# Kernel tuning notes

Measured on AMD Instinct MI355X. Metric: run time of the kernel, lower is better.

The kernel has to match this reference:

```python
import jax, jax.numpy as jnp
import numpy as np

# ---- fixed sizes ----
N_IN = 100_000          # total inner nodes
NODES_PER_INNER = 50    # nodes per inner graph
N_OUT = N_IN // NODES_PER_INNER          # 2000 outer nodes (= num inner graphs)
NODES_PER_OUTER = 125   # outer nodes per outer graph
B = N_OUT // NODES_PER_OUTER             # 16 graphs in the batch
DEG = 8
E_IN = N_IN * DEG        # 800_000 inner edges
E_OUT = N_OUT * DEG      # 16_000 outer edges
IN_FEATS = 64
OUT_FEATS = 64
H = 128                  # h_feats = [128]*6
NUM_CLASSES = 10


def _rand_edges(key, n_graphs, nodes_per_graph, edges_per_graph):
    """Random edges that stay inside each graph of a batched graph."""
    k1, k2 = jax.random.split(key)
    src_l = jax.random.randint(k1, (n_graphs, edges_per_graph), 0, nodes_per_graph)
    dst_l = jax.random.randint(k2, (n_graphs, edges_per_graph), 0, nodes_per_graph)
    off = (jnp.arange(n_graphs) * nodes_per_graph)[:, None]
    return ((src_l + off).reshape(-1).astype(jnp.int32),
            (dst_l + off).reshape(-1).astype(jnp.int32))


def setup_inputs() -> dict:
    key = jax.random.key(0)
    ks = jax.random.split(key, 24)
    inner_src, inner_dst = _rand_edges(ks[0], N_OUT, NODES_PER_INNER, E_IN // N_OUT)
    outer_src, outer_dst = _rand_edges(ks[1], B, NODES_PER_OUTER, E_OUT // B)

    def w(k, fan_in, fan_out):
        return jax.random.normal(k, (fan_in, fan_out), jnp.float32) * (1.0 / np.sqrt(fan_in))

    inp = {
        "in_layer_feat": jax.random.normal(ks[2], (N_IN, IN_FEATS), jnp.float32),
        "out_layer_feat": jax.random.normal(ks[3], (N_OUT, OUT_FEATS), jnp.float32),
        "inner_ew": jax.random.uniform(ks[4], (E_IN,), jnp.float32) + 0.5,
        "outer_ew": jax.random.uniform(ks[5], (E_OUT,), jnp.float32) + 0.5,
        "W1": w(ks[6], IN_FEATS, H),        "b1": jnp.zeros((H,), jnp.float32),
        "W2": w(ks[7], H, H),               "b2": jnp.zeros((H,), jnp.float32),
        "W3": w(ks[8], OUT_FEATS + H, H),   "b3": jnp.zeros((H,), jnp.float32),
        "W4": w(ks[9], H, H),               "b4": jnp.zeros((H,), jnp.float32),
        "W5": w(ks[10], H, H),              "b5": jnp.zeros((H,), jnp.float32),
        "W6": w(ks[11], H, H),              "b6": jnp.zeros((H,), jnp.float32),
        "Wc": w(ks[12], H, NUM_CLASSES),    "bc": jnp.zeros((NUM_CLASSES,), jnp.float32),
        "inner_src": inner_src, "inner_dst": inner_dst,
        "outer_src": outer_src, "outer_dst": outer_dst,
        "inner_node_graph": (jnp.arange(N_IN) // NODES_PER_INNER).astype(jnp.int32),
        "outer_node_graph": (jnp.arange(N_OUT) // NODES_PER_OUTER).astype(jnp.int32),
    }
    return inp


def graph_conv(src, dst, ew, x, W, b, n_nodes):
    """DGL GraphConv, norm='both', weighted aggregation, zero-in-degree allowed."""
    ones = jnp.ones(src.shape[0], x.dtype)
    deg_out = jnp.clip(jax.ops.segment_sum(ones, src, num_segments=n_nodes), 1.0)
    deg_in = jnp.clip(jax.ops.segment_sum(ones, dst, num_segments=n_nodes), 1.0)
    xs = x * jax.lax.rsqrt(deg_out)[:, None]                      # src normalization
    msg = xs[src] * ew[:, None]                                   # u_mul_e
    agg = jax.ops.segment_sum(msg, dst, num_segments=n_nodes)     # copy_e -> sum
    agg = agg * jax.lax.rsqrt(deg_in)[:, None]                    # dst normalization
    return agg @ W + b


def mean_nodes(h, node_graph, n_graphs, nodes_per_graph):
    return jax.ops.segment_sum(h, node_graph, num_segments=n_graphs) / nodes_per_graph


def reference(in_layer_feat, out_layer_feat, inner_ew, outer_ew,
              W1, b1, W2, b2, W3, b3, W4, b4, W5, b5, W6, b6, Wc, bc,
              inner_src, inner_dst, outer_src, outer_dst,
              inner_node_graph, outer_node_graph):
    # inner-graph message passing
    h = jax.nn.relu(graph_conv(inner_src, inner_dst, inner_ew, in_layer_feat, W1, b1, N_IN))
    h = jax.nn.relu(graph_conv(inner_src, inner_dst, inner_ew, h, W2, b2, N_IN))
    reduced = mean_nodes(h, inner_node_graph, N_OUT, float(NODES_PER_INNER))  # [N_OUT, H]
    merged = jnp.concatenate([out_layer_feat, reduced], axis=-1)              # [N_OUT, OUT_FEATS+H]
    # outer-graph message passing
    h = jax.nn.relu(graph_conv(outer_src, outer_dst, outer_ew, merged, W3, b3, N_OUT))
    h = jax.nn.relu(graph_conv(outer_src, outer_dst, outer_ew, h, W4, b4, N_OUT))
    h = jax.nn.relu(graph_conv(outer_src, outer_dst, outer_ew, h, W5, b5, N_OUT))
    h = jax.nn.relu(graph_conv(outer_src, outer_dst, outer_ew, h, W6, b6, N_OUT))
    hg = mean_nodes(h, outer_node_graph, B, float(NODES_PER_OUTER))           # [B, H]
    return hg @ Wc + bc                                                       # [B, NUM_CLASSES]
```

## Files before the change

kernel.cpp:

```cpp
#include <hip/hip_runtime.h>

#define NPI 50
#define EPI 400
#define NPO 125
#define EPO 1000
#define N_IN 100000
#define N_OUT 2000
#define NB 16
#define NC 10

typedef _Float16 half_t;
typedef _Float16 f16x8 __attribute__((ext_vector_type(8)));
typedef float f32x4 __attribute__((ext_vector_type(4)));

#define MFMA(a, b, c) __builtin_amdgcn_mfma_f32_16x16x32_f16(a, b, c, 0, 0, 0)

__device__ __forceinline__ void lds_barrier() {
    asm volatile("s_waitcnt lgkmcnt(0)" ::: "memory");
    __builtin_amdgcn_s_barrier();
}

__device__ __forceinline__ f16x8 lds_ld8(const half_t* base, int row, int k, int strideB) {
    return *(const f16x8*)((const char*)base + row * strideB + ((k * 2) ^ ((row & 7) << 4)));
}
__device__ __forceinline__ void lds_st1(half_t* base, int row, int col, int strideB, float v) {
    *(half_t*)((char*)base + row * strideB + ((col * 2) ^ ((row & 7) << 4))) = (half_t)v;
}
__device__ __forceinline__ void lds_st1h(half_t* base, int row, int col, int strideB, half_t v) {
    *(half_t*)((char*)base + row * strideB + ((col * 2) ^ ((row & 7) << 4))) = v;
}
__device__ __forceinline__ f16x8 scr_ld8(const half_t* base, int row, int k) {
    return *(const f16x8*)((const char*)base + row * 64 + ((k * 2) ^ ((row & 3) << 4)));
}
__device__ __forceinline__ void scr_st1(half_t* base, int row, int col, float v) {
    *(half_t*)((char*)base + row * 64 + ((col * 2) ^ ((row & 3) << 4))) = (half_t)v;
}

__global__ __launch_bounds__(256) void k_pre(
    const float* __restrict__ W1, const float* __restrict__ W2,
    const float* __restrict__ W3, const float* __restrict__ W4,
    const float* __restrict__ W5, const float* __restrict__ W6,
    half_t* __restrict__ WT1, half_t* __restrict__ WT2,
    half_t* __restrict__ WT3, half_t* __restrict__ WT4,
    half_t* __restrict__ WT5, half_t* __restrict__ WT6,
    const float* __restrict__ ew, const int* __restrict__ esrc,
    const int* __restrict__ edst, half_t* __restrict__ Aout)
{
    __shared__ float Af[NPO * NPO];
    __shared__ int cO[NPO], cI[NPO];
    __shared__ float rso[NPO], rsi[NPO];
    const int t = threadIdx.x;

    if (blockIdx.x < 384) {
        int i = blockIdx.x * 256 + t;
        const float* src; half_t* dst; int K;
        if      (i < 8192)  { src = W1; dst = WT1; K = 64; }
        else if (i < 24576) { src = W2; dst = WT2; K = 128; i -= 8192; }
        else if (i < 49152) { src = W3; dst = WT3; K = 192; i -= 24576; }
        else if (i < 65536) { src = W4; dst = WT4; K = 128; i -= 49152; }
        else if (i < 81920) { src = W5; dst = WT5; K = 128; i -= 65536; }
        else                { src = W6; dst = WT6; K = 128; i -= 81920; }
        int c = i & 127, k = i >> 7;
        dst[c * K + k] = (half_t)src[k * 128 + c];
        return;
    }

    const int g = blockIdx.x - 384;
    const int nb = g * NPO, eb = g * EPO;
    for (int i = t; i < NPO * NPO; i += 256) Af[i] = 0.f;
    if (t < NPO) { cO[t] = 0; cI[t] = 0; }
    __syncthreads();
    for (int e = t; e < EPO; e += 256) {
        int s = esrc[eb + e] - nb, d = edst[eb + e] - nb;
        atomicAdd(&Af[d * NPO + s], ew[eb + e]);
        atomicAdd(&cO[s], 1); atomicAdd(&cI[d], 1);
    }
    __syncthreads();
    if (t < NPO) {
        rso[t] = rsqrtf((float)max(cO[t], 1));
        rsi[t] = rsqrtf((float)max(cI[t], 1));
    }
    __syncthreads();
    for (int i = t; i < 128 * 16; i += 256) {
        int d = i >> 4, s0 = (i & 15) * 8;
        f16x8 v;
        #pragma unroll
        for (int j = 0; j < 8; j++) {
            int s = s0 + j;
            float x = (d < NPO && s < NPO) ? Af[d * NPO + s] * rsi[d] * rso[s] : 0.f;
            v[j] = (half_t)x;
        }
        *(f16x8*)&Aout[(size_t)g * 16384 + d * 128 + s0] = v;
    }
}

__global__ __launch_bounds__(256, 5) void k_inner(
    const float* __restrict__ X, const float* __restrict__ outfeat,
    const float* __restrict__ ew, const int* __restrict__ esrc,
    const int* __restrict__ edst,
    const half_t* __restrict__ WT1, const float* __restrict__ b1,
    const half_t* __restrict__ WT2, const float* __restrict__ b2,
    half_t* __restrict__ merged)
{
    __shared__ alignas(16) char smem[21504];
    half_t* R2  = (half_t*)smem;
    float*  Af  = (float*)smem;
    half_t* scr = (half_t*)(smem + 16384);
    float*  pool= (float*)(smem + 20480);
    int*    cO  = (int*)(smem + 20992);
    int*    cI  = (int*)(smem + 21248);

    const int g = blockIdx.x, t = threadIdx.x;
    const int w = t >> 6, l = t & 63, lr = l & 15, lk = l >> 4;
    const int nb = g * NPI, eb = g * EPI;
    half_t* scrw = scr + w * 512;

    float ofv = (t < 64) ? outfeat[(size_t)g * 64 + t] : 0.f;
    int s0e, d0e; float w0e;
    { int e = eb + t; s0e = esrc[e] - nb; d0e = edst[e] - nb; w0e = ew[e]; }
    int s1e = 0, d1e = 0; float w1e = 0.f;
    const bool e1v = (t + 256 < EPI);
    if (e1v) { int e = eb + t + 256; s1e = esrc[e] - nb; d1e = edst[e] - nb; w1e = ew[e]; }
    const int srow = t >> 2, qc = t & 3;
    f16x8 xh0 = {}, xh1 = {};
    if (srow < NPI) {
        const float* xp = &X[(size_t)(nb + srow) * 64 + qc * 16];
        float4 a = *(const float4*)(xp + 0), b = *(const float4*)(xp + 4);
        float4 c = *(const float4*)(xp + 8), d = *(const float4*)(xp + 12);
        xh0[0]=(half_t)a.x; xh0[1]=(half_t)a.y; xh0[2]=(half_t)a.z; xh0[3]=(half_t)a.w;
        xh0[4]=(half_t)b.x; xh0[5]=(half_t)b.y; xh0[6]=(half_t)b.z; xh0[7]=(half_t)b.w;
        xh1[0]=(half_t)c.x; xh1[1]=(half_t)c.y; xh1[2]=(half_t)c.z; xh1[3]=(half_t)c.w;
        xh1[4]=(half_t)d.x; xh1[5]=(half_t)d.y; xh1[6]=(half_t)d.z; xh1[7]=(half_t)d.w;
    }

    if (t < 64) { cO[t] = 0; cI[t] = 0; }
    if (t >= 64 && t < 192) pool[t - 64] = 0.f;
    for (int i = t; i < 4096; i += 256) Af[i] = 0.f;
    lds_barrier();

    atomicAdd(&Af[d0e * 64 + (s0e ^ ((d0e & 7) << 2))], w0e);
    atomicAdd(&cO[s0e], 1); atomicAdd(&cI[d0e], 1);
    if (e1v) {
        atomicAdd(&Af[d1e * 64 + (s1e ^ ((d1e & 7) << 2))], w1e);
        atomicAdd(&cO[s1e], 1); atomicAdd(&cI[d1e], 1);
    }
    lds_barrier();

    f16x8 afr[2];
    {
        const int r = w * 16 + lr;
        const int sw = (r & 7) << 2;
        const float rsi_l = rsqrtf((float)max(cI[r], 1));
        #pragma unroll
        for (int ks = 0; ks < 2; ks++) {
            const int c0 = ks * 32 + lk * 8;
            f32x4 v0 = *(const f32x4*)&Af[r * 64 + (c0 ^ sw)];
            f32x4 v1 = *(const f32x4*)&Af[r * 64 + ((c0 + 4) ^ sw)];
            f16x8 fr;
            #pragma unroll
            for (int j = 0; j < 4; j++)
                fr[j] = (half_t)(v0[j] * rsi_l * rsqrtf((float)max(cO[c0 + j], 1)));
            #pragma unroll
            for (int j = 0; j < 4; j++)
                fr[4 + j] = (half_t)(v1[j] * rsi_l * rsqrtf((float)max(cO[c0 + 4 + j], 1)));
            afr[ks] = fr;
        }
    }
    lds_barrier();

    #pragma unroll
    for (int i = 0; i < 8; i++) lds_st1h(R2, qc * 16 + i, srow, 128, xh0[i]);
    #pragma unroll
    for (int i = 0; i < 8; i++) lds_st1h(R2, qc * 16 + 8 + i, srow, 128, xh1[i]);
    lds_barrier();

    f32x4 hacc[8] = {};
    #pragma unroll
    for (int kf = 0; kf < 2; kf++) {
        f16x8 wb[8];
        #pragma unroll
        for (int nt = 0; nt < 8; nt++)
            wb[nt] = *(const f16x8*)&WT1[(nt * 16 + lr) * 64 + kf * 32 + lk * 8];
        #pragma unroll
        for (int j = 0; j < 2; j++) {
            const int ft = kf * 2 + j;
            f32x4 tacc = {};
            #pragma unroll
            for (int ks = 0; ks < 2; ks++) {
                f16x8 b = lds_ld8(R2, ft * 16 + lr, ks * 32 + lk * 8, 128);
                tacc = MFMA(afr[ks], b, tacc);
            }
            #pragma unroll
            for (int q = 0; q < 4; q++) scr_st1(scrw, lk * 4 + q, j * 16 + lr, tacc[q]);
        }
        f16x8 a1 = scr_ld8(scrw, lr, lk * 8);
        #pragma unroll
        for (int nt = 0; nt < 8; nt++) hacc[nt] = MFMA(a1, wb[nt], hacc[nt]);
    }
    lds_barrier();
    #pragma unroll
    for (int nt = 0; nt < 8; nt++) {
        int c = nt * 16 + lr;
        float bb = b1[c];
        #pragma unroll
        for (int q = 0; q < 4; q++)
            lds_st1(R2, c, w * 16 + lk * 4 + q, 128, fmaxf(hacc[nt][q] + bb, 0.f));
    }
    lds_barrier();

    f32x4 h2[8] = {};
    #pragma unroll
    for (int kf = 0; kf < 4; kf++) {
        f16x8 wb[8];
        #pragma unroll
        for (int nt = 0; nt < 8; nt++)
            wb[nt] = *(const f16x8*)&WT2[(nt * 16 + lr) * 128 + kf * 32 + lk * 8];
        #pragma unroll
        for (int j = 0; j < 2; j++) {
            const int ft = kf * 2 + j;
            f32x4 tacc = {};
            #pragma unroll
            for (int ks = 0; ks < 2; ks++) {
                f16x8 b = lds_ld8(R2, ft * 16 + lr, ks * 32 + lk * 8, 128);
                tacc = MFMA(afr[ks], b, tacc);
            }
            #pragma unroll
            for (int q = 0; q < 4; q++) scr_st1(scrw, lk * 4 + q, j * 16 + lr, tacc[q]);
        }
        f16x8 a1 = scr_ld8(scrw, lr, lk * 8);
        #pragma unroll
        for (int nt = 0; nt < 8; nt++) h2[nt] = MFMA(a1, wb[nt], h2[nt]);
    }
    #pragma unroll
    for (int nt = 0; nt < 8; nt++) {
        int c = nt * 16 + lr;
        float bb = b2[c];
        float ps = 0.f;
        #pragma unroll
        for (int q = 0; q < 4; q++) {
            int m = w * 16 + lk * 4 + q;
            float v = fmaxf(h2[nt][q] + bb, 0.f);
            ps += (m < NPI) ? v : 0.f;
        }
        ps += __shfl_xor(ps, 16);
        ps += __shfl_xor(ps, 32);
        if (lk == 0) atomicAdd(&pool[c], ps);
    }
    lds_barrier();
    if (t < 64) merged[(size_t)g * 192 + t] = (half_t)ofv;
    else if (t < 192) merged[(size_t)g * 192 + t] = (half_t)(pool[t - 64] * (1.f / NPI));
}

template <int FIN, bool STAGE, bool LAST>
__device__ __forceinline__ void outer_layer(
    const f16x8* afr, const half_t* __restrict__ mg,
    const half_t* __restrict__ WT, const float* __restrict__ bias,
    half_t* bufP, half_t* bufQ, float* pool,
    int wr, int wc, int lr, int lk, int t)
{
    f32x4 hacc[4] = {};
    constexpr int NCH = FIN / 64;
    f16x8 hv[NCH];
    if constexpr (STAGE) {
        const int s = t >> 3, fo = (t & 7) * 8;
        #pragma unroll
        for (int ch = 0; ch < NCH; ch++) {
            f16x8 z = {};
            hv[ch] = (s < NPO) ? *(const f16x8*)&mg[(size_t)s * 192 + ch * 64 + fo] : z;
        }
    }
    #pragma unroll
    for (int ch = 0; ch < NCH; ch++) {
        f16x8 wtb[8];
        #pragma unroll
        for (int ks2 = 0; ks2 < 2; ks2++)
            #pragma unroll
            for (int nt = 0; nt < 4; nt++)
                wtb[ks2 * 4 + nt] = *(const f16x8*)&WT[
                    (size_t)(wc * 64 + nt * 16 + lr) * FIN + ch * 64 + ks2 * 32 + lk * 8];
        if constexpr (STAGE) {
            const int s = t >> 3, fo = (t & 7) * 8;
            #pragma unroll
            for (int j = 0; j < 8; j++) lds_st1h(bufP, fo + j, s, 256, hv[ch][j]);
            lds_barrier();
        }
        const int rb = STAGE ? 0 : ch * 64;
        f32x4 tacc[2] = {};
        #pragma unroll
        for (int ks = 0; ks < 4; ks++) {
            #pragma unroll
            for (int nt = 0; nt < 2; nt++) {
                f16x8 b = lds_ld8(bufP, rb + wc * 32 + nt * 16 + lr, ks * 32 + lk * 8, 256);
                tacc[nt] = MFMA(afr[ks], b, tacc[nt]);
            }
        }
        #pragma unroll
        for (int nt = 0; nt < 2; nt++)
            #pragma unroll
            for (int q = 0; q < 4; q++)
                lds_st1(bufQ, wr * 16 + lk * 4 + q, wc * 32 + nt * 16 + lr, 128,
                        tacc[nt][q]);
        lds_barrier();
        #pragma unroll
        for (int ks2 = 0; ks2 < 2; ks2++) {
            f16x8 a1 = lds_ld8(bufQ, wr * 16 + lr, ks2 * 32 + lk * 8, 128);
            #pragma unroll
            for (int nt = 0; nt < 4; nt++)
                hacc[nt] = MFMA(a1, wtb[ks2 * 4 + nt], hacc[nt]);
        }
        lds_barrier();
    }
    if constexpr (!LAST) {
        #pragma unroll
        for (int nt = 0; nt < 4; nt++) {
            int c = wc * 64 + nt * 16 + lr;
            float bb = bias[c];
            #pragma unroll
            for (int q = 0; q < 4; q++)
                lds_st1(bufP, c, wr * 16 + lk * 4 + q, 256, fmaxf(hacc[nt][q] + bb, 0.f));
        }
        lds_barrier();
    } else {
        #pragma unroll
        for (int nt = 0; nt < 4; nt++) {
            int c = wc * 64 + nt * 16 + lr;
            float bb = bias[c];
            float ps = 0.f;
            #pragma unroll
            for (int q = 0; q < 4; q++) {
                int d = wr * 16 + lk * 4 + q;
                float v = fmaxf(hacc[nt][q] + bb, 0.f);
                ps += (d < NPO) ? v : 0.f;
            }
            ps += __shfl_xor(ps, 16);
            ps += __shfl_xor(ps, 32);
            if (lk == 0) atomicAdd(&pool[c], ps);
        }
        lds_barrier();
    }
}

__global__ __launch_bounds__(1024) void k_outer(
    const half_t* __restrict__ Aout, const half_t* __restrict__ merged,
    const half_t* __restrict__ WT3, const float* __restrict__ b3,
    const half_t* __restrict__ WT4, const float* __restrict__ b4,
    const half_t* __restrict__ WT5, const float* __restrict__ b5,
    const half_t* __restrict__ WT6, const float* __restrict__ b6,
    const float* __restrict__ Wc, const float* __restrict__ bc,
    float* __restrict__ out)
{
    __shared__ alignas(16) char smem[49704];
    half_t* bufP = (half_t*)smem;
    half_t* bufQ = (half_t*)(smem + 32768);
    float*  pool = (float*)(smem + 49152);
    float*  cls  = (float*)(smem + 49664);

    const int g = blockIdx.x, t = threadIdx.x;
    const int w = t >> 6, l = t & 63, lr = l & 15, lk = l >> 4;
    const int wr = w & 7, wc = w >> 3;
    const half_t* mg = merged + (size_t)g * NPO * 192;

    f16x8 afr[4];
    #pragma unroll
    for (int ks = 0; ks < 4; ks++)
        afr[ks] = *(const f16x8*)&Aout[(size_t)g * 16384
                                       + (wr * 16 + lr) * 128 + ks * 32 + lk * 8];
    if (t < 128) pool[t] = 0.f;
    if (t >= 128 && t < 128 + NC) cls[t - 128] = 0.f;
    lds_barrier();

    outer_layer<192, true,  false>(afr, mg, WT3, b3, bufP, bufQ, pool, wr, wc, lr, lk, t);
    outer_layer<128, false, false>(afr, nullptr, WT4, b4, bufP, bufQ, pool, wr, wc, lr, lk, t);
    outer_layer<128, false, false>(afr, nullptr, WT5, b5, bufP, bufQ, pool, wr, wc, lr, lk, t);
    outer_layer<128, false, true >(afr, nullptr, WT6, b6, bufP, bufQ, pool, wr, wc, lr, lk, t);

    if (t < 128) {
        float val = pool[t] * (1.f / NPO);
        float p[NC];
        #pragma unroll
        for (int c = 0; c < NC; c++) p[c] = val * Wc[t * NC + c];
        #pragma unroll
        for (int off = 32; off >= 1; off >>= 1)
            #pragma unroll
            for (int c = 0; c < NC; c++) p[c] += __shfl_xor(p[c], off);
        if ((t & 63) == 0)
            #pragma unroll
            for (int c = 0; c < NC; c++) atomicAdd(&cls[c], p[c]);
    }
    lds_barrier();
    if (t < NC) out[g * NC + t] = cls[t] + bc[t];
}

extern "C" void kernel_launch(void* const* d_in, const int* in_sizes, int n_in,
                              void* d_out, int out_size, void* d_ws, size_t ws_size,
                              hipStream_t stream)
{
    const float* X       = (const float*)d_in[0];
    const float* outfeat = (const float*)d_in[1];
    const float* iew     = (const float*)d_in[2];
    const float* oew     = (const float*)d_in[3];
    const float* W1 = (const float*)d_in[4];  const float* b1 = (const float*)d_in[5];
    const float* W2 = (const float*)d_in[6];  const float* b2 = (const float*)d_in[7];
    const float* W3 = (const float*)d_in[8];  const float* b3 = (const float*)d_in[9];
    const float* W4 = (const float*)d_in[10]; const float* b4 = (const float*)d_in[11];
    const float* W5 = (const float*)d_in[12]; const float* b5 = (const float*)d_in[13];
    const float* W6 = (const float*)d_in[14]; const float* b6 = (const float*)d_in[15];
    const float* Wc = (const float*)d_in[16]; const float* bc = (const float*)d_in[17];
    const int* isrc = (const int*)d_in[18];   const int* idst = (const int*)d_in[19];
    const int* osrc = (const int*)d_in[20];   const int* odst = (const int*)d_in[21];

    char* base = (char*)d_ws;
    half_t* WT1 = (half_t*)(base + 0);
    half_t* WT2 = (half_t*)(base + 16384);
    half_t* WT3 = (half_t*)(base + 49152);
    half_t* WT4 = (half_t*)(base + 98304);
    half_t* WT5 = (half_t*)(base + 131072);
    half_t* WT6 = (half_t*)(base + 163840);
    half_t* AoutG  = (half_t*)(base + 196608);
    half_t* merged = (half_t*)(base + 720896);

    k_pre<<<400, 256, 0, stream>>>(W1, W2, W3, W4, W5, W6,
                                   WT1, WT2, WT3, WT4, WT5, WT6,
                                   oew, osrc, odst, AoutG);
    k_inner<<<N_OUT, 256, 0, stream>>>(X, outfeat, iew, isrc, idst,
                                       WT1, b1, WT2, b2, merged);
    k_outer<<<NB, 1024, 0, stream>>>(AoutG, merged, WT3, b3, WT4, b4,
                                     WT5, b5, WT6, b6, Wc, bc, (float*)d_out);
}
```

Before: 122.0 us.

## Split outer-graph stage into per-layer multi-block kernels with transposed activations

Replaces the single outer-graph kernel, which ran 16 blocks of 1024 threads over all four layers, with four per-layer kernels of 128 single-wave blocks plus a small pooling and classifier kernel. Each block handles a 16-row slice of one outer graph and reads the previous layer's transposed fp16 activations from global memory. The inner kernel now writes the merged features in this transposed per-graph layout. The aim is to spread the outer stage across many more compute units instead of 16. The cost is four extra kernel launches, global round-trips between layers, and padding columns of the transposed merged buffer that are never initialised.

```diff
diff --git a/kernel.cpp b/kernel.cpp
--- a/kernel.cpp
+++ b/kernel.cpp
@@ -29,11 +29,11 @@
 __device__ __forceinline__ void lds_st1h(half_t* base, int row, int col, int strideB, half_t v) {
     *(half_t*)((char*)base + row * strideB + ((col * 2) ^ ((row & 7) << 4))) = v;
 }
-__device__ __forceinline__ f16x8 scr_ld8(const half_t* base, int row, int k) {
-    return *(const f16x8*)((const char*)base + row * 64 + ((k * 2) ^ ((row & 3) << 4)));
-}
-__device__ __forceinline__ void scr_st1(half_t* base, int row, int col, float v) {
-    *(half_t*)((char*)base + row * 64 + ((col * 2) ^ ((row & 3) << 4))) = (half_t)v;
+__device__ __forceinline__ f16x8 scrS_ld8(const half_t* base, int row, int k, int strideB) {
+    return *(const f16x8*)((const char*)base + row * strideB + ((k * 2) ^ ((row & 3) << 4)));
+}
+__device__ __forceinline__ void scrS_st1(half_t* base, int row, int col, int strideB, float v) {
+    *(half_t*)((char*)base + row * strideB + ((col * 2) ^ ((row & 3) << 4))) = (half_t)v;
 }
 
 __global__ __launch_bounds__(256) void k_pre(
@@ -100,7 +100,7 @@
     const int* __restrict__ edst,
     const half_t* __restrict__ WT1, const float* __restrict__ b1,
     const half_t* __restrict__ WT2, const float* __restrict__ b2,
-    half_t* __restrict__ merged)
+    half_t* __restrict__ mergedT)
 {
     __shared__ alignas(16) char smem[21504];
     half_t* R2  = (half_t*)smem;
@@ -191,9 +191,9 @@
                 tacc = MFMA(afr[ks], b, tacc);
             }
             #pragma unroll
-            for (int q = 0; q < 4; q++) scr_st1(scrw, lk * 4 + q, j * 16 + lr, tacc[q]);
-        }
-        f16x8 a1 = scr_ld8(scrw, lr, lk * 8);
+            for (int q = 0; q < 4; q++) scrS_st1(scrw, lk * 4 + q, j * 16 + lr, 64, tacc[q]);
+        }
+        f16x8 a1 = scrS_ld8(scrw, lr, lk * 8, 64);
         #pragma unroll
         for (int nt = 0; nt < 8; nt++) hacc[nt] = MFMA(a1, wb[nt], hacc[nt]);
     }
@@ -225,9 +225,9 @@
                 tacc = MFMA(afr[ks], b, tacc);
             }
             #pragma unroll
-            for (int q = 0; q < 4; q++) scr_st1(scrw, lk * 4 + q, j * 16 + lr, tacc[q]);
-        }
-        f16x8 a1 = scr_ld8(scrw, lr, lk * 8);
+            for (int q = 0; q < 4; q++) scrS_st1(scrw, lk * 4 + q, j * 16 + lr, 64, tacc[q]);
+        }
+        f16x8 a1 = scrS_ld8(scrw, lr, lk * 8, 64);
         #pragma unroll
         for (int nt = 0; nt < 8; nt++) h2[nt] = MFMA(a1, wb[nt], h2[nt]);
     }
@@ -247,135 +247,93 @@
         if (lk == 0) atomicAdd(&pool[c], ps);
     }
     lds_barrier();
-    if (t < 64) merged[(size_t)g * 192 + t] = (half_t)ofv;
-    else if (t < 192) merged[(size_t)g * 192 + t] = (half_t)(pool[t - 64] * (1.f / NPI));
-}
-
-template <int FIN, bool STAGE, bool LAST>
-__device__ __forceinline__ void outer_layer(
-    const f16x8* afr, const half_t* __restrict__ mg,
+    {
+        const int og = g / NPO, n = g - og * NPO;
+        half_t* mT = mergedT + (size_t)og * 192 * 128 + n;
+        if (t < 64) mT[(size_t)t * 128] = (half_t)ofv;
+        else if (t < 192) mT[(size_t)t * 128] = (half_t)(pool[t - 64] * (1.f / NPI));
+    }
+}
+
+template <int FIN>
+__global__ __launch_bounds__(64) void k_layer(
+    const half_t* __restrict__ Aout, const half_t* __restrict__ inT,
     const half_t* __restrict__ WT, const float* __restrict__ bias,
-    half_t* bufP, half_t* bufQ, float* pool,
-    int wr, int wc, int lr, int lk, int t)
-{
-    f32x4 hacc[4] = {};
-    constexpr int NCH = FIN / 64;
-    f16x8 hv[NCH];
-    if constexpr (STAGE) {
-        const int s = t >> 3, fo = (t & 7) * 8;
-        #pragma unroll
-        for (int ch = 0; ch < NCH; ch++) {
-            f16x8 z = {};
-            hv[ch] = (s < NPO) ? *(const f16x8*)&mg[(size_t)s * 192 + ch * 64 + fo] : z;
-        }
-    }
-    #pragma unroll
-    for (int ch = 0; ch < NCH; ch++) {
-        f16x8 wtb[8];
-        #pragma unroll
-        for (int ks2 = 0; ks2 < 2; ks2++)
-            #pragma unroll
-            for (int nt = 0; nt < 4; nt++)
-                wtb[ks2 * 4 + nt] = *(const f16x8*)&WT[
-                    (size_t)(wc * 64 + nt * 16 + lr) * FIN + ch * 64 + ks2 * 32 + lk * 8];
-        if constexpr (STAGE) {
-            const int s = t >> 3, fo = (t & 7) * 8;
-            #pragma unroll
-            for (int j = 0; j < 8; j++) lds_st1h(bufP, fo + j, s, 256, hv[ch][j]);
-            lds_barrier();
-        }
-        const int rb = STAGE ? 0 : ch * 64;
-        f32x4 tacc[2] = {};
+    half_t* __restrict__ outT)
+{
+    __shared__ alignas(16) half_t scrT[16 * FIN];
+    __shared__ alignas(16) half_t hts[128 * 16];
+    const int t = threadIdx.x, lr = t & 15, lk = t >> 4;
+    const int og = blockIdx.x >> 3, r0 = (blockIdx.x & 7) * 16;
+    const half_t* Ag = Aout + (size_t)og * 16384;
+    const half_t* ig = inT + (size_t)og * FIN * 128;
+
+    f16x8 af[4];
+    #pragma unroll
+    for (int ks = 0; ks < 4; ks++)
+        af[ks] = *(const f16x8*)&Ag[(size_t)(r0 + lr) * 128 + ks * 32 + lk * 8];
+
+    constexpr int NT = FIN / 16;
+    #pragma unroll
+    for (int nt = 0; nt < NT; nt++) {
+        f32x4 tacc = {};
         #pragma unroll
         for (int ks = 0; ks < 4; ks++) {
-            #pragma unroll
-            for (int nt = 0; nt < 2; nt++) {
-                f16x8 b = lds_ld8(bufP, rb + wc * 32 + nt * 16 + lr, ks * 32 + lk * 8, 256);
-                tacc[nt] = MFMA(afr[ks], b, tacc[nt]);
-            }
-        }
-        #pragma unroll
-        for (int nt = 0; nt < 2; nt++)
-            #pragma unroll
-            for (int q = 0; q < 4; q++)
-                lds_st1(bufQ, wr * 16 + lk * 4 + q, wc * 32 + nt * 16 + lr, 128,
-                        tacc[nt][q]);
-        lds_barrier();
-        #pragma unroll
-        for (int ks2 = 0; ks2 < 2; ks2++) {
-            f16x8 a1 = lds_ld8(bufQ, wr * 16 + lr, ks2 * 32 + lk * 8, 128);
-            #pragma unroll
-            for (int nt = 0; nt < 4; nt++)
-                hacc[nt] = MFMA(a1, wtb[ks2 * 4 + nt], hacc[nt]);
-        }
-        lds_barrier();
-    }
-    if constexpr (!LAST) {
-        #pragma unroll
-        for (int nt = 0; nt < 4; nt++) {
-            int c = wc * 64 + nt * 16 + lr;
-            float bb = bias[c];
-            #pragma unroll
-            for (int q = 0; q < 4; q++)
-                lds_st1(bufP, c, wr * 16 + lk * 4 + q, 256, fmaxf(hacc[nt][q] + bb, 0.f));
-        }
-        lds_barrier();
-    } else {
-        #pragma unroll
-        for (int nt = 0; nt < 4; nt++) {
-            int c = wc * 64 + nt * 16 + lr;
-            float bb = bias[c];
-            float ps = 0.f;
-            #pragma unroll
-            for (int q = 0; q < 4; q++) {
-                int d = wr * 16 + lk * 4 + q;
-                float v = fmaxf(hacc[nt][q] + bb, 0.f);
-                ps += (d < NPO) ? v : 0.f;
-            }
-            ps += __shfl_xor(ps, 16);
-            ps += __shfl_xor(ps, 32);
-            if (lk == 0) atomicAdd(&pool[c], ps);
-        }
-        lds_barrier();
-    }
-}
-
-__global__ __launch_bounds__(1024) void k_outer(
-    const half_t* __restrict__ Aout, const half_t* __restrict__ merged,
-    const half_t* __restrict__ WT3, const float* __restrict__ b3,
-    const half_t* __restrict__ WT4, const float* __restrict__ b4,
-    const half_t* __restrict__ WT5, const float* __restrict__ b5,
-    const half_t* __restrict__ WT6, const float* __restrict__ b6,
-    const float* __restrict__ Wc, const float* __restrict__ bc,
-    float* __restrict__ out)
-{
-    __shared__ alignas(16) char smem[49704];
-    half_t* bufP = (half_t*)smem;
-    half_t* bufQ = (half_t*)(smem + 32768);
-    float*  pool = (float*)(smem + 49152);
-    float*  cls  = (float*)(smem + 49664);
-
-    const int g = blockIdx.x, t = threadIdx.x;
-    const int w = t >> 6, l = t & 63, lr = l & 15, lk = l >> 4;
-    const int wr = w & 7, wc = w >> 3;
-    const half_t* mg = merged + (size_t)g * NPO * 192;
-
-    f16x8 afr[4];
-    #pragma unroll
-    for (int ks = 0; ks < 4; ks++)
-        afr[ks] = *(const f16x8*)&Aout[(size_t)g * 16384
-                                       + (wr * 16 + lr) * 128 + ks * 32 + lk * 8];
-    if (t < 128) pool[t] = 0.f;
-    if (t >= 128 && t < 128 + NC) cls[t - 128] = 0.f;
-    lds_barrier();
-
-    outer_layer<192, true,  false>(afr, mg, WT3, b3, bufP, bufQ, pool, wr, wc, lr, lk, t);
-    outer_layer<128, false, false>(afr, nullptr, WT4, b4, bufP, bufQ, pool, wr, wc, lr, lk, t);
-    outer_layer<128, false, false>(afr, nullptr, WT5, b5, bufP, bufQ, pool, wr, wc, lr, lk, t);
-    outer_layer<128, false, true >(afr, nullptr, WT6, b6, bufP, bufQ, pool, wr, wc, lr, lk, t);
-
-    if (t < 128) {
-        float val = pool[t] * (1.f / NPO);
+            f16x8 b = *(const f16x8*)&ig[(size_t)(nt * 16 + lr) * 128 + ks * 32 + lk * 8];
+            tacc = MFMA(af[ks], b, tacc);
+        }
+        #pragma unroll
+        for (int q = 0; q < 4; q++)
+            scrS_st1(scrT, lk * 4 + q, nt * 16 + lr, FIN * 2, tacc[q]);
+    }
+
+    f32x4 hacc[8] = {};
+    #pragma unroll
+    for (int ks2 = 0; ks2 < FIN / 32; ks2++) {
+        f16x8 a1 = scrS_ld8(scrT, lr, ks2 * 32 + lk * 8, FIN * 2);
+        #pragma unroll
+        for (int nt2 = 0; nt2 < 8; nt2++) {
+            f16x8 wb = *(const f16x8*)&WT[(size_t)(nt2 * 16 + lr) * FIN + ks2 * 32 + lk * 8];
+            hacc[nt2] = MFMA(a1, wb, hacc[nt2]);
+        }
+    }
+    #pragma unroll
+    for (int nt2 = 0; nt2 < 8; nt2++) {
+        int c = nt2 * 16 + lr;
+        float bb = bias[c];
+        #pragma unroll
+        for (int q = 0; q < 4; q++)
+            hts[c * 16 + lk * 4 + q] = (half_t)fmaxf(hacc[nt2][q] + bb, 0.f);
+    }
+    #pragma unroll
+    for (int j = 0; j < 4; j++) {
+        int id = t + j * 64;
+        int f = id >> 1, i0 = (id & 1) * 8;
+        f16x8 v = *(const f16x8*)&hts[f * 16 + i0];
+        *(f16x8*)&outT[(size_t)og * 16384 + (size_t)f * 128 + r0 + i0] = v;
+    }
+}
+
+__global__ __launch_bounds__(128) void k_pool(
+    const half_t* __restrict__ h6T, const float* __restrict__ Wc,
+    const float* __restrict__ bc, float* __restrict__ out)
+{
+    __shared__ float cls[NC];
+    const int og = blockIdx.x, t = threadIdx.x;
+    if (t < NC) cls[t] = 0.f;
+    const half_t* hp = h6T + (size_t)og * 16384 + (size_t)t * 128;
+    float s = 0.f;
+    #pragma unroll
+    for (int i = 0; i < 15; i++) {
+        f16x8 v = *(const f16x8*)&hp[i * 8];
+        #pragma unroll
+        for (int j = 0; j < 8; j++) s += (float)v[j];
+    }
+    #pragma unroll
+    for (int i = 120; i < 125; i++) s += (float)hp[i];
+    const float val = s * (1.f / NPO);
+    __syncthreads();
+    {
         float p[NC];
         #pragma unroll
         for (int c = 0; c < NC; c++) p[c] = val * Wc[t * NC + c];
@@ -387,8 +345,8 @@
             #pragma unroll
             for (int c = 0; c < NC; c++) atomicAdd(&cls[c], p[c]);
     }
-    lds_barrier();
-    if (t < NC) out[g * NC + t] = cls[t] + bc[t];
+    __syncthreads();
+    if (t < NC) out[og * NC + t] = cls[t] + bc[t];
 }
 
 extern "C" void kernel_launch(void* const* d_in, const int* in_sizes, int n_in,
@@ -416,14 +374,19 @@
     half_t* WT4 = (half_t*)(base + 98304);
     half_t* WT5 = (half_t*)(base + 131072);
     half_t* WT6 = (half_t*)(base + 163840);
-    half_t* AoutG  = (half_t*)(base + 196608);
-    half_t* merged = (half_t*)(base + 720896);
+    half_t* AoutG   = (half_t*)(base + 196608);
+    half_t* mergedT = (half_t*)(base + 720896);
+    half_t* hTa     = (half_t*)(base + 1507328);
+    half_t* hTb     = (half_t*)(base + 2031616);
 
     k_pre<<<400, 256, 0, stream>>>(W1, W2, W3, W4, W5, W6,
                                    WT1, WT2, WT3, WT4, WT5, WT6,
                                    oew, osrc, odst, AoutG);
     k_inner<<<N_OUT, 256, 0, stream>>>(X, outfeat, iew, isrc, idst,
-                                       WT1, b1, WT2, b2, merged);
-    k_outer<<<NB, 1024, 0, stream>>>(AoutG, merged, WT3, b3, WT4, b4,
-                                     WT5, b5, WT6, b6, Wc, bc, (float*)d_out);
-}
+                                       WT1, b1, WT2, b2, mergedT);
+    k_layer<192><<<NB * 8, 64, 0, stream>>>(AoutG, mergedT, WT3, b3, hTa);
+    k_layer<128><<<NB * 8, 64, 0, stream>>>(AoutG, hTa, WT4, b4, hTb);
+    k_layer<128><<<NB * 8, 64, 0, stream>>>(AoutG, hTb, WT5, b5, hTa);
+    k_layer<128><<<NB * 8, 64, 0, stream>>>(AoutG, hTa, WT6, b6, hTb);
+    k_pool<<<NB, 128, 0, stream>>>(hTb, Wc, bc, (float*)d_out);
+}
```

Measured after the change: 135.3 us. +10.9%, slower.
